# Optimization experiments

Measured on AMD Instinct MI355X. Metric: run time of the kernel, lower is better.

Reference implementation:

```python
import jax, jax.numpy as jnp
import numpy as np

IN_DIM = 768
D_MODEL = 256
B, T = 64, 2048
LN_EPS = 1e-5


def setup_inputs() -> dict:
    key = jax.random.key(0)
    ks = jax.random.split(key, 8)
    s_in = 1.0 / np.sqrt(IN_DIM)
    s_d = 1.0 / np.sqrt(D_MODEL)
    return {
        "x": jax.random.normal(ks[0], (B, T, IN_DIM), dtype=jnp.float32),
        "ln_gamma": jnp.ones((IN_DIM,), jnp.float32),
        "ln_beta": jnp.zeros((IN_DIM,), jnp.float32),
        "W_proj": jax.random.uniform(ks[1], (IN_DIM, D_MODEL), jnp.float32, -s_in, s_in),
        "b_proj": jax.random.uniform(ks[2], (D_MODEL,), jnp.float32, -s_in, s_in),
        "W1": jax.random.uniform(ks[3], (D_MODEL, D_MODEL), jnp.float32, -s_d, s_d),
        "b1": jax.random.uniform(ks[4], (D_MODEL,), jnp.float32, -s_d, s_d),
        "W2": jax.random.uniform(ks[5], (D_MODEL,), jnp.float32, -s_d, s_d),
        "b2": jax.random.uniform(ks[6], (), jnp.float32, -s_d, s_d),
    }


def reference(x, ln_gamma, ln_beta, W_proj, b_proj, W1, b1, W2, b2):
    # nan/inf sanitization to 0
    x = jnp.nan_to_num(x, nan=0.0, posinf=0.0, neginf=0.0)
    # LayerNorm over last dim (biased variance, eps=1e-5)
    mu = jnp.mean(x, axis=-1, keepdims=True)
    var = jnp.mean(jnp.square(x - mu), axis=-1, keepdims=True)
    xn = (x - mu) * jax.lax.rsqrt(var + LN_EPS) * ln_gamma + ln_beta
    # projection to d_model: [B, T, D]
    h = jnp.einsum('btf,fd->btd', xn, W_proj) + b_proj
    # tanh-MLP attention scores: [B, T]
    a = jnp.tanh(jnp.einsum('btd,de->bte', h, W1) + b1)
    w = jnp.einsum('bte,e->bt', a, W2) + b2
    w = jax.nn.softmax(w, axis=-1)
    # weighted-sum pooling over T: [B, D]
    return jnp.einsum('btd,bt->bd', h, w)
```

## Files before the change

kernel.cpp:

```cpp
#include <hip/hip_runtime.h>

#define LN_EPS 1e-5f

typedef __attribute__((ext_vector_type(8))) short s8vec;
typedef __attribute__((ext_vector_type(4))) float f4vec;

#define OFF_WPF   0u
#define OFF_W1F   393216u
#define OFF_U     524288u
#define OFF_C     525312u
#define OFF_UPART 526336u
#define OFF_VPART 575488u
#define OFF_PM    624640u
#define OFF_PS    632832u
#define OFF_PO    641024u

#define BAR()     asm volatile("s_barrier" ::: "memory")
#define WAIT_L0() asm volatile("s_waitcnt lgkmcnt(0)" ::: "memory")

__device__ __forceinline__ unsigned short f2bf(float f) {
  unsigned int u = __float_as_uint(f);
  u += 0x7fffu + ((u >> 16) & 1u);
  return (unsigned short)(u >> 16);
}
__device__ __forceinline__ float bf2f(unsigned short h) {
  return __uint_as_float(((unsigned int)h) << 16);
}

__global__ void k0_prep(const float* __restrict__ Wp,
                        const float* __restrict__ gamma,
                        const float* __restrict__ beta,
                        const float* __restrict__ W1,
                        char* __restrict__ ws) {
  const int blk = blockIdx.x;
  const int n = threadIdx.x;
  if (blk < 48) {
    unsigned short* wpf = (unsigned short*)(ws + OFF_WPF);
    const int wid = n >> 6, nn = (n >> 4) & 3, lr = n & 15;
    const int k0 = blk * 16;
    float up = 0.f, vp = 0.f;
#pragma unroll
    for (int j = 0; j < 16; ++j) {
      const int k = k0 + j;
      const float w = Wp[k * 256 + n];
      const float wpv = gamma[k] * w;
      up += wpv;
      vp += beta[k] * w;
      const int c = k >> 6, ks = (k >> 5) & 1, lqd = (k >> 3) & 3, jj = k & 7;
      wpf[(((((c * 4 + wid) * 2 + ks) * 4 + nn) * 64) + lqd * 16 + lr) * 8 + jj] = f2bf(wpv);
    }
    ((float*)(ws + OFF_UPART))[blk * 256 + n] = up;
    ((float*)(ws + OFF_VPART))[blk * 256 + n] = vp;
  } else {
    unsigned short* w1f = (unsigned short*)(ws + OFF_W1F);
    const int d0 = (blk - 48) * 16;
    const int t = n >> 4, lre = n & 15;
#pragma unroll
    for (int jj = 0; jj < 16; ++jj) {
      const int d = d0 + jj;
      const int ks = d >> 5, lqd = (d >> 3) & 3, j = d & 7;
      w1f[(((t * 8 + ks) * 64) + lqd * 16 + lre) * 8 + j] = f2bf(W1[d * 256 + n]);
    }
  }
}

__global__ void k0_reduce(const float* __restrict__ bproj, char* __restrict__ ws) {
  const int n = threadIdx.x;
  const float* upart = (const float*)(ws + OFF_UPART);
  const float* vpart = (const float*)(ws + OFF_VPART);
  float u = 0.f, v = 0.f;
  for (int i = 0; i < 48; ++i) {
    u += upart[i * 256 + n];
    v += vpart[i * 256 + n];
  }
  ((float*)(ws + OFF_U))[n] = u;
  ((float*)(ws + OFF_C))[n] = v + bproj[n];
}

__global__ __launch_bounds__(256)
void k1_main(const float* __restrict__ x,
             const float* __restrict__ b1,
             const float* __restrict__ W2,
             char* __restrict__ ws) {
  __shared__ __align__(16) char sm[36864];
  char* const sm_h = sm;
  float* const f_b1 = (float*)(sm + 32768);
  float* const f_w2 = (float*)(sm + 33792);
  float* const f_lp = (float*)(sm + 34816);
  float* const f_lg = (float*)(sm + 35840);
  float* const f_e  = (float*)(sm + 36096);
  float* const f_mu = (float*)(sm + 36352);
  float* const f_iv = (float*)(sm + 36608);

  const int tid  = threadIdx.x;
  const int lane = tid & 63;
  const int wid  = tid >> 6;
  const int lr = lane & 15;
  const int lq = lane >> 4;

  const int arow = tid >> 2;
  const int aq   = tid & 3;
  const float* xrow = x + (size_t)(blockIdx.x * 64 + arow) * 768 + aq * 16;

  const char* wpf = (const char*)ws + OFF_WPF + wid * 8192 + lane * 16;

  const f4vec fz = {0.f, 0.f, 0.f, 0.f};
  f4vec acc[4][4];
#pragma unroll
  for (int m = 0; m < 4; ++m)
#pragma unroll
    for (int n = 0; n < 4; ++n) acc[m][n] = fz;

  float s1 = 0.f, s2 = 0.f;
  float xv[16];

  auto loadx = [&](int c) {
#pragma unroll
    for (int j = 0; j < 4; ++j) {
      const float4 t = *(const float4*)(xrow + c * 64 + j * 4);
      xv[4*j+0] = t.x; xv[4*j+1] = t.y; xv[4*j+2] = t.z; xv[4*j+3] = t.w;
    }
  };
  auto packA = [&](int p) {
    unsigned int pk[8];
#pragma unroll
    for (int j = 0; j < 16; ++j) {
      float f = xv[j];
      if ((__float_as_uint(f) & 0x7f800000u) == 0x7f800000u) f = 0.f;
      s1 += f; s2 += f * f;
      const unsigned int hb = f2bf(f);
      if ((j & 1) == 0) pk[j >> 1] = hb; else pk[j >> 1] |= hb << 16;
    }
    const int base = arow * 128 + aq * 32;
    const int sw = (arow & 7) << 4;
    char* ab = sm + p * 8192;
    *(int4*)(ab + ((base     ) ^ sw)) = make_int4((int)pk[0], (int)pk[1], (int)pk[2], (int)pk[3]);
    *(int4*)(ab + ((base + 16) ^ sw)) = make_int4((int)pk[4], (int)pk[5], (int)pk[6], (int)pk[7]);
  };

  loadx(0);
  packA(0);
  loadx(1);
  WAIT_L0(); BAR();

  for (int c = 0; c < 12; ++c) {
    s8vec bfv[8];
#pragma unroll
    for (int ks = 0; ks < 2; ++ks)
#pragma unroll
      for (int n = 0; n < 4; ++n)
        bfv[ks * 4 + n] =
            *(const s8vec*)(wpf + (size_t)(((c * 4) * 2 + ks) * 4 + n) * 1024);
    if (c < 11) packA((c + 1) & 1);
    if (c < 10) loadx(c + 2);
#pragma unroll
    for (int ks = 0; ks < 2; ++ks) {
      const int kb = (ks * 32 + lq * 8) * 2;
      s8vec af[4];
#pragma unroll
      for (int m = 0; m < 4; ++m) {
        const int row = m * 16 + lr;
        af[m] = *(const s8vec*)(sm + (c & 1) * 8192 + ((row * 128 + kb) ^ ((row & 7) << 4)));
      }
#pragma unroll
      for (int m = 0; m < 4; ++m)
#pragma unroll
        for (int n = 0; n < 4; ++n)
          acc[m][n] = __builtin_amdgcn_mfma_f32_16x16x32_bf16(af[m], bfv[ks * 4 + n], acc[m][n], 0, 0, 0);
    }
    WAIT_L0();
    BAR();
  }

  s1 += __shfl_xor(s1, 1); s1 += __shfl_xor(s1, 2);
  s2 += __shfl_xor(s2, 1); s2 += __shfl_xor(s2, 2);
  if (aq == 0) {
    const float mu = s1 * (1.f / 768.f);
    float var = s2 * (1.f / 768.f) - mu * mu;
    var = fmaxf(var, 0.f);
    f_mu[arow] = mu;
    f_iv[arow] = rsqrtf(var + LN_EPS);
  }
  f_b1[tid] = b1[tid];
  f_w2[tid] = W2[tid];
  float u4[4], c4[4];
#pragma unroll
  for (int n = 0; n < 4; ++n) {
    u4[n] = ((const float*)(ws + OFF_U))[wid * 64 + n * 16 + lr];
    c4[n] = ((const float*)(ws + OFF_C))[wid * 64 + n * 16 + lr];
  }
  WAIT_L0();
  BAR();

#pragma unroll
  for (int m = 0; m < 4; ++m) {
#pragma unroll
    for (int i = 0; i < 4; ++i) {
      const int rl = m * 16 + lq * 4 + i;
      const float mu  = f_mu[rl];
      const float inv = f_iv[rl];
      const int sw = (rl & 7) << 4;
#pragma unroll
      for (int n = 0; n < 4; ++n) {
        const int cd = wid * 64 + n * 16 + lr;
        const float h = inv * (acc[m][n][i] - mu * u4[n]) + c4[n];
        *(unsigned short*)(sm_h + ((rl * 512 + cd * 2) ^ sw)) = f2bf(h);
      }
    }
  }
  WAIT_L0();
  BAR();

  const char* w1f = (const char*)ws + OFF_W1F;
  f4vec acc2[4][4];
#pragma unroll
  for (int m = 0; m < 4; ++m)
#pragma unroll
    for (int n = 0; n < 4; ++n) acc2[m][n] = fz;

#pragma unroll
  for (int ks = 0; ks < 8; ++ks) {
    s8vec af[4], bf[4];
#pragma unroll
    for (int et = 0; et < 4; ++et)
      af[et] = *(const s8vec*)(w1f + (((wid * 4 + et) * 8 + ks) * 64 + lane) * 16);
#pragma unroll
    for (int rt = 0; rt < 4; ++rt) {
      const int r = rt * 16 + lr;
      bf[rt] = *(const s8vec*)(sm_h + ((r * 512 + ks * 64 + lq * 16) ^ ((r & 7) << 4)));
    }
#pragma unroll
    for (int et = 0; et < 4; ++et)
#pragma unroll
      for (int rt = 0; rt < 4; ++rt)
        acc2[et][rt] = __builtin_amdgcn_mfma_f32_16x16x32_bf16(af[et], bf[rt], acc2[et][rt], 0, 0, 0);
  }

  float lp[4] = {0.f, 0.f, 0.f, 0.f};
#pragma unroll
  for (int et = 0; et < 4; ++et) {
#pragma unroll
    for (int i = 0; i < 4; ++i) {
      const int e = wid * 64 + et * 16 + lq * 4 + i;
      const float b1v = f_b1[e];
      const float w2v = f_w2[e];
#pragma unroll
      for (int rt = 0; rt < 4; ++rt) {
        float z = acc2[et][rt][i] + b1v;
        z = fminf(fmaxf(z, -15.f), 15.f);
        const float e2 = __expf(2.f * z);
        const float a = (e2 - 1.f) / (e2 + 1.f);
        lp[rt] += a * w2v;
      }
    }
  }
#pragma unroll
  for (int rt = 0; rt < 4; ++rt) {
    float t = lp[rt];
    t += __shfl_xor(t, 16);
    t += __shfl_xor(t, 32);
    if (lq == 0) f_lp[(rt * 16 + lr) * 4 + wid] = t;
  }
  __syncthreads();
  if (tid < 64)
    f_lg[tid] = f_lp[tid*4+0] + f_lp[tid*4+1] + f_lp[tid*4+2] + f_lp[tid*4+3];
  __syncthreads();

  float mx = -1e30f;
  for (int r = 0; r < 64; ++r) mx = fmaxf(mx, f_lg[r]);
  if (tid < 64) f_e[tid] = __expf(f_lg[tid] - mx);
  __syncthreads();

  {
    const int d = tid;
    float o = 0.f;
    for (int r = 0; r < 64; ++r) {
      const float ev = f_e[r];
      const unsigned short hb =
          *(const unsigned short*)(sm_h + ((r * 512 + d * 2) ^ ((r & 7) << 4)));
      o += ev * bf2f(hb);
    }
    ((float*)(ws + OFF_PO))[blockIdx.x * 256 + d] = o;
  }
  if (tid == 0) {
    float s = 0.f;
    for (int r = 0; r < 64; ++r) s += f_e[r];
    ((float*)(ws + OFF_PS))[blockIdx.x] = s;
    ((float*)(ws + OFF_PM))[blockIdx.x] = mx;
  }
}

__global__ void k2_combine(const char* __restrict__ ws, float* __restrict__ out) {
  const int b = blockIdx.x;
  const int d = threadIdx.x;
  const float* pm = (const float*)(ws + OFF_PM) + b * 32;
  const float* ps = (const float*)(ws + OFF_PS) + b * 32;
  const float* po = (const float*)(ws + OFF_PO) + (size_t)b * 32 * 256;
  float mx = -1e30f;
  for (int c = 0; c < 32; ++c) mx = fmaxf(mx, pm[c]);
  float num = 0.f, den = 0.f;
  for (int c = 0; c < 32; ++c) {
    const float al = __expf(pm[c] - mx);
    den += al * ps[c];
    num += al * po[c * 256 + d];
  }
  out[b * 256 + d] = num / den;
}

extern "C" void kernel_launch(void* const* d_in, const int* in_sizes, int n_in,
                              void* d_out, int out_size, void* d_ws, size_t ws_size,
                              hipStream_t stream) {
  const float* x     = (const float*)d_in[0];
  const float* gamma = (const float*)d_in[1];
  const float* beta  = (const float*)d_in[2];
  const float* Wp    = (const float*)d_in[3];
  const float* bproj = (const float*)d_in[4];
  const float* W1    = (const float*)d_in[5];
  const float* b1    = (const float*)d_in[6];
  const float* W2    = (const float*)d_in[7];
  char* ws = (char*)d_ws;
  float* out = (float*)d_out;

  k0_prep   <<<dim3(64),   dim3(256), 0, stream>>>(Wp, gamma, beta, W1, ws);
  k0_reduce <<<dim3(1),    dim3(256), 0, stream>>>(bproj, ws);
  k1_main   <<<dim3(2048), dim3(256), 0, stream>>>(x, b1, W2, ws);
  k2_combine<<<dim3(64),   dim3(256), 0, stream>>>(ws, out);
}
```

Baseline: 158.7 us.

## Halve rows per block to 32 and double grid for occupancy

```diff
diff --git a/kernel.cpp b/kernel.cpp
--- a/kernel.cpp
+++ b/kernel.cpp
@@ -12,8 +12,8 @@
 #define OFF_UPART 526336u
 #define OFF_VPART 575488u
 #define OFF_PM    624640u
-#define OFF_PS    632832u
-#define OFF_PO    641024u
+#define OFF_PS    641024u
+#define OFF_PO    657408u
 
 #define BAR()     asm volatile("s_barrier" ::: "memory")
 #define WAIT_L0() asm volatile("s_waitcnt lgkmcnt(0)" ::: "memory")
@@ -82,15 +82,15 @@
              const float* __restrict__ b1,
              const float* __restrict__ W2,
              char* __restrict__ ws) {
-  __shared__ __align__(16) char sm[36864];
+  __shared__ __align__(16) char sm[19456];
   char* const sm_h = sm;
-  float* const f_b1 = (float*)(sm + 32768);
-  float* const f_w2 = (float*)(sm + 33792);
-  float* const f_lp = (float*)(sm + 34816);
-  float* const f_lg = (float*)(sm + 35840);
-  float* const f_e  = (float*)(sm + 36096);
-  float* const f_mu = (float*)(sm + 36352);
-  float* const f_iv = (float*)(sm + 36608);
+  float* const f_b1 = (float*)(sm + 16384);
+  float* const f_w2 = (float*)(sm + 17408);
+  float* const f_lp = (float*)(sm + 18432);
+  float* const f_lg = (float*)(sm + 18944);
+  float* const f_e  = (float*)(sm + 19072);
+  float* const f_mu = (float*)(sm + 19200);
+  float* const f_iv = (float*)(sm + 19328);
 
   const int tid  = threadIdx.x;
   const int lane = tid & 63;
@@ -98,82 +98,86 @@
   const int lr = lane & 15;
   const int lq = lane >> 4;
 
-  const int arow = tid >> 2;
-  const int aq   = tid & 3;
-  const float* xrow = x + (size_t)(blockIdx.x * 64 + arow) * 768 + aq * 16;
+  const int arow = tid >> 3;
+  const int aq   = tid & 7;
+  const float* xrow = x + (size_t)(blockIdx.x * 32 + arow) * 768 + aq * 8;
 
   const char* wpf = (const char*)ws + OFF_WPF + wid * 8192 + lane * 16;
 
   const f4vec fz = {0.f, 0.f, 0.f, 0.f};
-  f4vec acc[4][4];
-#pragma unroll
-  for (int m = 0; m < 4; ++m)
+  f4vec acc[2][4];
+#pragma unroll
+  for (int m = 0; m < 2; ++m)
 #pragma unroll
     for (int n = 0; n < 4; ++n) acc[m][n] = fz;
 
   float s1 = 0.f, s2 = 0.f;
-  float xv[16];
-
-  auto loadx = [&](int c) {
-#pragma unroll
-    for (int j = 0; j < 4; ++j) {
+  float xvA[8], xvB[8];
+
+  auto loadx = [&](float (&xv)[8], int c) {
+#pragma unroll
+    for (int j = 0; j < 2; ++j) {
       const float4 t = *(const float4*)(xrow + c * 64 + j * 4);
       xv[4*j+0] = t.x; xv[4*j+1] = t.y; xv[4*j+2] = t.z; xv[4*j+3] = t.w;
     }
   };
-  auto packA = [&](int p) {
-    unsigned int pk[8];
-#pragma unroll
-    for (int j = 0; j < 16; ++j) {
+  auto packA = [&](const float (&xv)[8], int p) {
+    unsigned int pk[4];
+#pragma unroll
+    for (int j = 0; j < 8; ++j) {
       float f = xv[j];
       if ((__float_as_uint(f) & 0x7f800000u) == 0x7f800000u) f = 0.f;
       s1 += f; s2 += f * f;
       const unsigned int hb = f2bf(f);
       if ((j & 1) == 0) pk[j >> 1] = hb; else pk[j >> 1] |= hb << 16;
     }
-    const int base = arow * 128 + aq * 32;
-    const int sw = (arow & 7) << 4;
-    char* ab = sm + p * 8192;
-    *(int4*)(ab + ((base     ) ^ sw)) = make_int4((int)pk[0], (int)pk[1], (int)pk[2], (int)pk[3]);
-    *(int4*)(ab + ((base + 16) ^ sw)) = make_int4((int)pk[4], (int)pk[5], (int)pk[6], (int)pk[7]);
+    *(int4*)(sm + p * 4096 + ((arow * 128 + aq * 16) ^ ((arow & 7) << 4))) =
+        make_int4((int)pk[0], (int)pk[1], (int)pk[2], (int)pk[3]);
   };
-
-  loadx(0);
-  packA(0);
-  loadx(1);
-  WAIT_L0(); BAR();
-
-  for (int c = 0; c < 12; ++c) {
+  auto mfmaStep = [&](int c) {
     s8vec bfv[8];
 #pragma unroll
     for (int ks = 0; ks < 2; ++ks)
 #pragma unroll
       for (int n = 0; n < 4; ++n)
         bfv[ks * 4 + n] =
-            *(const s8vec*)(wpf + (size_t)(((c * 4) * 2 + ks) * 4 + n) * 1024);
-    if (c < 11) packA((c + 1) & 1);
-    if (c < 10) loadx(c + 2);
+            *(const s8vec*)(wpf + (size_t)(c * 32768 + ks * 4096 + n * 1024));
 #pragma unroll
     for (int ks = 0; ks < 2; ++ks) {
       const int kb = (ks * 32 + lq * 8) * 2;
-      s8vec af[4];
-#pragma unroll
-      for (int m = 0; m < 4; ++m) {
+      s8vec af[2];
+#pragma unroll
+      for (int m = 0; m < 2; ++m) {
         const int row = m * 16 + lr;
-        af[m] = *(const s8vec*)(sm + (c & 1) * 8192 + ((row * 128 + kb) ^ ((row & 7) << 4)));
+        af[m] = *(const s8vec*)(sm + (c & 1) * 4096 + ((row * 128 + kb) ^ ((row & 7) << 4)));
       }
 #pragma unroll
-      for (int m = 0; m < 4; ++m)
+      for (int m = 0; m < 2; ++m)
 #pragma unroll
         for (int n = 0; n < 4; ++n)
           acc[m][n] = __builtin_amdgcn_mfma_f32_16x16x32_bf16(af[m], bfv[ks * 4 + n], acc[m][n], 0, 0, 0);
     }
-    WAIT_L0();
-    BAR();
-  }
-
-  s1 += __shfl_xor(s1, 1); s1 += __shfl_xor(s1, 2);
-  s2 += __shfl_xor(s2, 1); s2 += __shfl_xor(s2, 2);
+  };
+
+  loadx(xvA, 0);
+  loadx(xvB, 1);
+  packA(xvA, 0);
+  loadx(xvA, 2);
+  WAIT_L0(); BAR();
+
+  for (int cc = 0; cc < 12; cc += 2) {
+    packA(xvB, 1);
+    if (cc + 3 <= 11) loadx(xvB, cc + 3);
+    mfmaStep(cc);
+    WAIT_L0(); BAR();
+    if (cc + 2 <= 11) packA(xvA, 0);
+    if (cc + 4 <= 11) loadx(xvA, cc + 4);
+    mfmaStep(cc + 1);
+    WAIT_L0(); BAR();
+  }
+
+  s1 += __shfl_xor(s1, 1); s1 += __shfl_xor(s1, 2); s1 += __shfl_xor(s1, 4);
+  s2 += __shfl_xor(s2, 1); s2 += __shfl_xor(s2, 2); s2 += __shfl_xor(s2, 4);
   if (aq == 0) {
     const float mu = s1 * (1.f / 768.f);
     float var = s2 * (1.f / 768.f) - mu * mu;
@@ -193,7 +197,7 @@
   BAR();
 
 #pragma unroll
-  for (int m = 0; m < 4; ++m) {
+  for (int m = 0; m < 2; ++m) {
 #pragma unroll
     for (int i = 0; i < 4; ++i) {
       const int rl = m * 16 + lq * 4 + i;
@@ -212,31 +216,31 @@
   BAR();
 
   const char* w1f = (const char*)ws + OFF_W1F;
-  f4vec acc2[4][4];
+  f4vec acc2[4][2];
 #pragma unroll
   for (int m = 0; m < 4; ++m)
 #pragma unroll
-    for (int n = 0; n < 4; ++n) acc2[m][n] = fz;
+    for (int n = 0; n < 2; ++n) acc2[m][n] = fz;
 
 #pragma unroll
   for (int ks = 0; ks < 8; ++ks) {
-    s8vec af[4], bf[4];
+    s8vec af[4], bf[2];
 #pragma unroll
     for (int et = 0; et < 4; ++et)
       af[et] = *(const s8vec*)(w1f + (((wid * 4 + et) * 8 + ks) * 64 + lane) * 16);
 #pragma unroll
-    for (int rt = 0; rt < 4; ++rt) {
+    for (int rt = 0; rt < 2; ++rt) {
       const int r = rt * 16 + lr;
       bf[rt] = *(const s8vec*)(sm_h + ((r * 512 + ks * 64 + lq * 16) ^ ((r & 7) << 4)));
     }
 #pragma unroll
     for (int et = 0; et < 4; ++et)
 #pragma unroll
-      for (int rt = 0; rt < 4; ++rt)
+      for (int rt = 0; rt < 2; ++rt)
         acc2[et][rt] = __builtin_amdgcn_mfma_f32_16x16x32_bf16(af[et], bf[rt], acc2[et][rt], 0, 0, 0);
   }
 
-  float lp[4] = {0.f, 0.f, 0.f, 0.f};
+  float lp[2] = {0.f, 0.f};
 #pragma unroll
   for (int et = 0; et < 4; ++et) {
 #pragma unroll
@@ -245,7 +249,7 @@
       const float b1v = f_b1[e];
       const float w2v = f_w2[e];
 #pragma unroll
-      for (int rt = 0; rt < 4; ++rt) {
+      for (int rt = 0; rt < 2; ++rt) {
         float z = acc2[et][rt][i] + b1v;
         z = fminf(fmaxf(z, -15.f), 15.f);
         const float e2 = __expf(2.f * z);
@@ -255,26 +259,26 @@
     }
   }
 #pragma unroll
-  for (int rt = 0; rt < 4; ++rt) {
+  for (int rt = 0; rt < 2; ++rt) {
     float t = lp[rt];
     t += __shfl_xor(t, 16);
     t += __shfl_xor(t, 32);
     if (lq == 0) f_lp[(rt * 16 + lr) * 4 + wid] = t;
   }
   __syncthreads();
-  if (tid < 64)
+  if (tid < 32)
     f_lg[tid] = f_lp[tid*4+0] + f_lp[tid*4+1] + f_lp[tid*4+2] + f_lp[tid*4+3];
   __syncthreads();
 
   float mx = -1e30f;
-  for (int r = 0; r < 64; ++r) mx = fmaxf(mx, f_lg[r]);
-  if (tid < 64) f_e[tid] = __expf(f_lg[tid] - mx);
+  for (int r = 0; r < 32; ++r) mx = fmaxf(mx, f_lg[r]);
+  if (tid < 32) f_e[tid] = __expf(f_lg[tid] - mx);
   __syncthreads();
 
   {
     const int d = tid;
     float o = 0.f;
-    for (int r = 0; r < 64; ++r) {
+    for (int r = 0; r < 32; ++r) {
       const float ev = f_e[r];
       const unsigned short hb =
           *(const unsigned short*)(sm_h + ((r * 512 + d * 2) ^ ((r & 7) << 4)));
@@ -284,7 +288,7 @@
   }
   if (tid == 0) {
     float s = 0.f;
-    for (int r = 0; r < 64; ++r) s += f_e[r];
+    for (int r = 0; r < 32; ++r) s += f_e[r];
     ((float*)(ws + OFF_PS))[blockIdx.x] = s;
     ((float*)(ws + OFF_PM))[blockIdx.x] = mx;
   }
@@ -293,13 +297,13 @@
 __global__ void k2_combine(const char* __restrict__ ws, float* __restrict__ out) {
   const int b = blockIdx.x;
   const int d = threadIdx.x;
-  const float* pm = (const float*)(ws + OFF_PM) + b * 32;
-  const float* ps = (const float*)(ws + OFF_PS) + b * 32;
-  const float* po = (const float*)(ws + OFF_PO) + (size_t)b * 32 * 256;
+  const float* pm = (const float*)(ws + OFF_PM) + b * 64;
+  const float* ps = (const float*)(ws + OFF_PS) + b * 64;
+  const float* po = (const float*)(ws + OFF_PO) + (size_t)b * 64 * 256;
   float mx = -1e30f;
-  for (int c = 0; c < 32; ++c) mx = fmaxf(mx, pm[c]);
+  for (int c = 0; c < 64; ++c) mx = fmaxf(mx, pm[c]);
   float num = 0.f, den = 0.f;
-  for (int c = 0; c < 32; ++c) {
+  for (int c = 0; c < 64; ++c) {
     const float al = __expf(pm[c] - mx);
     den += al * ps[c];
     num += al * po[c * 256 + d];
@@ -323,6 +327,6 @@
 
   k0_prep   <<<dim3(64),   dim3(256), 0, stream>>>(Wp, gamma, beta, W1, ws);
   k0_reduce <<<dim3(1),    dim3(256), 0, stream>>>(bproj, ws);
-  k1_main   <<<dim3(2048), dim3(256), 0, stream>>>(x, b1, W2, ws);
+  k1_main   <<<dim3(4096), dim3(256), 0, stream>>>(x, b1, W2, ws);
   k2_combine<<<dim3(64),   dim3(256), 0, stream>>>(ws, out);
 }
```

Measured after the change: 182.5 us. 1.15x slower.

## Give each wave its own 16 rows and all 256 columns, removing LDS staging of x

Applied to the files above, without the earlier changes.

```diff
diff --git a/kernel.cpp b/kernel.cpp
--- a/kernel.cpp
+++ b/kernel.cpp
@@ -5,7 +5,7 @@
 typedef __attribute__((ext_vector_type(8))) short s8vec;
 typedef __attribute__((ext_vector_type(4))) float f4vec;
 
-#define OFF_WPF   0u
+#define OFF_W2F   0u
 #define OFF_W1F   393216u
 #define OFF_U     524288u
 #define OFF_C     525312u
@@ -15,7 +15,6 @@
 #define OFF_PS    632832u
 #define OFF_PO    641024u
 
-#define BAR()     asm volatile("s_barrier" ::: "memory")
 #define WAIT_L0() asm volatile("s_waitcnt lgkmcnt(0)" ::: "memory")
 
 __device__ __forceinline__ unsigned short f2bf(float f) {
@@ -35,8 +34,8 @@
   const int blk = blockIdx.x;
   const int n = threadIdx.x;
   if (blk < 48) {
-    unsigned short* wpf = (unsigned short*)(ws + OFF_WPF);
-    const int wid = n >> 6, nn = (n >> 4) & 3, lr = n & 15;
+    unsigned short* w2f = (unsigned short*)(ws + OFF_W2F);
+    const int nt = n >> 4, lr = n & 15;
     const int k0 = blk * 16;
     float up = 0.f, vp = 0.f;
 #pragma unroll
@@ -46,8 +45,8 @@
       const float wpv = gamma[k] * w;
       up += wpv;
       vp += beta[k] * w;
-      const int c = k >> 6, ks = (k >> 5) & 1, lqd = (k >> 3) & 3, jj = k & 7;
-      wpf[(((((c * 4 + wid) * 2 + ks) * 4 + nn) * 64) + lqd * 16 + lr) * 8 + jj] = f2bf(wpv);
+      const int c = k >> 5, lqd = (k >> 3) & 3, jj = k & 7;
+      w2f[(((c * 16 + nt) * 64) + lqd * 16 + lr) * 8 + jj] = f2bf(wpv);
     }
     ((float*)(ws + OFF_UPART))[blk * 256 + n] = up;
     ((float*)(ws + OFF_VPART))[blk * 256 + n] = vp;
@@ -82,15 +81,17 @@
              const float* __restrict__ b1,
              const float* __restrict__ W2,
              char* __restrict__ ws) {
-  __shared__ __align__(16) char sm[36864];
-  char* const sm_h = sm;
-  float* const f_b1 = (float*)(sm + 32768);
-  float* const f_w2 = (float*)(sm + 33792);
-  float* const f_lp = (float*)(sm + 34816);
-  float* const f_lg = (float*)(sm + 35840);
-  float* const f_e  = (float*)(sm + 36096);
-  float* const f_mu = (float*)(sm + 36352);
-  float* const f_iv = (float*)(sm + 36608);
+  __shared__ __align__(16) char sm[38912];
+  char* const sm_h  = sm;
+  float* const f_u  = (float*)(sm + 32768);
+  float* const f_c  = (float*)(sm + 33792);
+  float* const f_b1 = (float*)(sm + 34816);
+  float* const f_w2 = (float*)(sm + 35840);
+  float* const f_lp = (float*)(sm + 36864);
+  float* const f_lg = (float*)(sm + 37888);
+  float* const f_e  = (float*)(sm + 38144);
+  float* const f_mu = (float*)(sm + 38400);
+  float* const f_iv = (float*)(sm + 38656);
 
   const int tid  = threadIdx.x;
   const int lane = tid & 63;
@@ -98,118 +99,94 @@
   const int lr = lane & 15;
   const int lq = lane >> 4;
 
-  const int arow = tid >> 2;
-  const int aq   = tid & 3;
-  const float* xrow = x + (size_t)(blockIdx.x * 64 + arow) * 768 + aq * 16;
-
-  const char* wpf = (const char*)ws + OFF_WPF + wid * 8192 + lane * 16;
+  f_u[tid]  = ((const float*)(ws + OFF_U))[tid];
+  f_c[tid]  = ((const float*)(ws + OFF_C))[tid];
+  f_b1[tid] = b1[tid];
+  f_w2[tid] = W2[tid];
+  __syncthreads();
+
+  const float* xrow = x + (size_t)(blockIdx.x * 64 + wid * 16 + lr) * 768 + lq * 8;
+  const char* w2f = (const char*)ws + OFF_W2F;
 
   const f4vec fz = {0.f, 0.f, 0.f, 0.f};
-  f4vec acc[4][4];
-#pragma unroll
-  for (int m = 0; m < 4; ++m)
-#pragma unroll
-    for (int n = 0; n < 4; ++n) acc[m][n] = fz;
+  f4vec acc[16];
+#pragma unroll
+  for (int nt = 0; nt < 16; ++nt) acc[nt] = fz;
 
   float s1 = 0.f, s2 = 0.f;
-  float xv[16];
-
-  auto loadx = [&](int c) {
-#pragma unroll
-    for (int j = 0; j < 4; ++j) {
-      const float4 t = *(const float4*)(xrow + c * 64 + j * 4);
-      xv[4*j+0] = t.x; xv[4*j+1] = t.y; xv[4*j+2] = t.z; xv[4*j+3] = t.w;
-    }
+  float xvA[8], xvB[8];
+
+  auto loadx = [&](float (&xv)[8], int c) {
+    const float4 t0 = *(const float4*)(xrow + c * 32);
+    const float4 t1 = *(const float4*)(xrow + c * 32 + 4);
+    xv[0]=t0.x; xv[1]=t0.y; xv[2]=t0.z; xv[3]=t0.w;
+    xv[4]=t1.x; xv[5]=t1.y; xv[6]=t1.z; xv[7]=t1.w;
   };
-  auto packA = [&](int p) {
-    unsigned int pk[8];
-#pragma unroll
-    for (int j = 0; j < 16; ++j) {
+  auto packA = [&](const float (&xv)[8]) -> s8vec {
+    unsigned int pk[4];
+#pragma unroll
+    for (int j = 0; j < 8; ++j) {
       float f = xv[j];
       if ((__float_as_uint(f) & 0x7f800000u) == 0x7f800000u) f = 0.f;
       s1 += f; s2 += f * f;
       const unsigned int hb = f2bf(f);
       if ((j & 1) == 0) pk[j >> 1] = hb; else pk[j >> 1] |= hb << 16;
     }
-    const int base = arow * 128 + aq * 32;
-    const int sw = (arow & 7) << 4;
-    char* ab = sm + p * 8192;
-    *(int4*)(ab + ((base     ) ^ sw)) = make_int4((int)pk[0], (int)pk[1], (int)pk[2], (int)pk[3]);
-    *(int4*)(ab + ((base + 16) ^ sw)) = make_int4((int)pk[4], (int)pk[5], (int)pk[6], (int)pk[7]);
+    return *(s8vec*)pk;
   };
-
-  loadx(0);
-  packA(0);
-  loadx(1);
-  WAIT_L0(); BAR();
-
-  for (int c = 0; c < 12; ++c) {
-    s8vec bfv[8];
-#pragma unroll
-    for (int ks = 0; ks < 2; ++ks)
-#pragma unroll
-      for (int n = 0; n < 4; ++n)
-        bfv[ks * 4 + n] =
-            *(const s8vec*)(wpf + (size_t)(((c * 4) * 2 + ks) * 4 + n) * 1024);
-    if (c < 11) packA((c + 1) & 1);
-    if (c < 10) loadx(c + 2);
-#pragma unroll
-    for (int ks = 0; ks < 2; ++ks) {
-      const int kb = (ks * 32 + lq * 8) * 2;
-      s8vec af[4];
-#pragma unroll
-      for (int m = 0; m < 4; ++m) {
-        const int row = m * 16 + lr;
-        af[m] = *(const s8vec*)(sm + (c & 1) * 8192 + ((row * 128 + kb) ^ ((row & 7) << 4)));
-      }
-#pragma unroll
-      for (int m = 0; m < 4; ++m)
-#pragma unroll
-        for (int n = 0; n < 4; ++n)
-          acc[m][n] = __builtin_amdgcn_mfma_f32_16x16x32_bf16(af[m], bfv[ks * 4 + n], acc[m][n], 0, 0, 0);
-    }
-    WAIT_L0();
-    BAR();
-  }
-
-  s1 += __shfl_xor(s1, 1); s1 += __shfl_xor(s1, 2);
-  s2 += __shfl_xor(s2, 1); s2 += __shfl_xor(s2, 2);
-  if (aq == 0) {
+  auto mfmaChunk = [&](int c, s8vec af) {
+#pragma unroll
+    for (int g = 0; g < 4; ++g) {
+      s8vec bfv[4];
+#pragma unroll
+      for (int t = 0; t < 4; ++t)
+        bfv[t] = *(const s8vec*)(w2f + ((size_t)(c * 16 + g * 4 + t) * 64 + lane) * 16);
+#pragma unroll
+      for (int t = 0; t < 4; ++t)
+        acc[g * 4 + t] = __builtin_amdgcn_mfma_f32_16x16x32_bf16(af, bfv[t], acc[g * 4 + t], 0, 0, 0);
+    }
+  };
+
+  loadx(xvA, 0);
+  loadx(xvB, 1);
+  for (int cc = 0; cc < 24; cc += 2) {
+    const s8vec afA = packA(xvA);
+    if (cc + 2 < 24) loadx(xvA, cc + 2);
+    mfmaChunk(cc, afA);
+    const s8vec afB = packA(xvB);
+    if (cc + 3 < 24) loadx(xvB, cc + 3);
+    mfmaChunk(cc + 1, afB);
+  }
+
+  s1 += __shfl_xor(s1, 16); s1 += __shfl_xor(s1, 32);
+  s2 += __shfl_xor(s2, 16); s2 += __shfl_xor(s2, 32);
+  if (lane < 16) {
     const float mu = s1 * (1.f / 768.f);
     float var = s2 * (1.f / 768.f) - mu * mu;
     var = fmaxf(var, 0.f);
-    f_mu[arow] = mu;
-    f_iv[arow] = rsqrtf(var + LN_EPS);
-  }
-  f_b1[tid] = b1[tid];
-  f_w2[tid] = W2[tid];
-  float u4[4], c4[4];
-#pragma unroll
-  for (int n = 0; n < 4; ++n) {
-    u4[n] = ((const float*)(ws + OFF_U))[wid * 64 + n * 16 + lr];
-    c4[n] = ((const float*)(ws + OFF_C))[wid * 64 + n * 16 + lr];
+    f_mu[wid * 16 + lr] = mu;
+    f_iv[wid * 16 + lr] = rsqrtf(var + LN_EPS);
   }
   WAIT_L0();
-  BAR();
-
-#pragma unroll
-  for (int m = 0; m < 4; ++m) {
+
+  float muv[4], ivv[4];
+#pragma unroll
+  for (int i = 0; i < 4; ++i) {
+    muv[i] = f_mu[wid * 16 + lq * 4 + i];
+    ivv[i] = f_iv[wid * 16 + lq * 4 + i];
+  }
+#pragma unroll
+  for (int nt = 0; nt < 16; ++nt) {
+    const int cd = nt * 16 + lr;
+    const float uv = f_u[cd], cv = f_c[cd];
 #pragma unroll
     for (int i = 0; i < 4; ++i) {
-      const int rl = m * 16 + lq * 4 + i;
-      const float mu  = f_mu[rl];
-      const float inv = f_iv[rl];
-      const int sw = (rl & 7) << 4;
-#pragma unroll
-      for (int n = 0; n < 4; ++n) {
-        const int cd = wid * 64 + n * 16 + lr;
-        const float h = inv * (acc[m][n][i] - mu * u4[n]) + c4[n];
-        *(unsigned short*)(sm_h + ((rl * 512 + cd * 2) ^ sw)) = f2bf(h);
-      }
-    }
-  }
-  WAIT_L0();
-  BAR();
+      const int rl = wid * 16 + lq * 4 + i;
+      const float h = ivv[i] * (acc[nt][i] - muv[i] * uv) + cv;
+      *(unsigned short*)(sm_h + ((rl * 512 + cd * 2) ^ ((rl & 7) << 4))) = f2bf(h);
+    }
+  }
+  __syncthreads();
 
   const char* w1f = (const char*)ws + OFF_W1F;
   f4vec acc2[4][4];
```

Result: slower. 256.2 us (+61.4%).
